# Kernel optimization log

Hardware: AMD Instinct MI355X
Metric: run time of the kernel (lower is better)

## Reference

```python
import jax, jax.numpy as jnp
import numpy as np

EMBED_DIM = 128
NUM_SYMBOLS = 100000
PAD_IDX = NUM_SYMBOLS
B = 8192
K = 50


def setup_inputs() -> dict:
    key = jax.random.key(0)
    ks = jax.random.split(key, 10)
    emb = jax.random.normal(ks[0], (NUM_SYMBOLS + 1, EMBED_DIM), jnp.float32) * 0.02
    emb = emb.at[PAD_IDX].set(0.0)  # padding_idx row is zero
    xav2 = 1.0 / np.sqrt(0.5 * (2 * EMBED_DIM + EMBED_DIM))
    xavg1 = 1.0 / np.sqrt(0.5 * (EMBED_DIM + EMBED_DIM // 2))
    xavg2 = 1.0 / np.sqrt(0.5 * (EMBED_DIM // 2 + 1))
    return {
        "entity": jax.random.randint(ks[1], (B,), 0, NUM_SYMBOLS),
        "connections": jax.random.randint(ks[2], (B, K, 2), 0, NUM_SYMBOLS),
        "symbol_emb": emb,
        "gcn_w_W": jax.random.normal(ks[3], (EMBED_DIM, 2 * EMBED_DIM), jnp.float32) * xav2,
        "gcn_w_b": jnp.zeros((EMBED_DIM,), jnp.float32),
        "gcn_b": jnp.zeros((EMBED_DIM,), jnp.float32),
        "gate_w1": jax.random.normal(ks[4], (EMBED_DIM // 2, EMBED_DIM), jnp.float32) * xavg1,
        "gate_b1": jnp.zeros((EMBED_DIM // 2,), jnp.float32),
        "gate_w2": jax.random.normal(ks[5], (1, EMBED_DIM // 2), jnp.float32) * xavg2,
        "gate_b2": jnp.zeros((1,), jnp.float32),
        "gate_temp": jnp.float32(1.0),
    }


def reference(entity, connections, symbol_emb, gcn_w_W, gcn_w_b, gcn_b,
              gate_w1, gate_b1, gate_w2, gate_b2, gate_temp):
    # Gather: center + (relation, entity) neighbor embeddings
    self_emb = symbol_emb[entity]                      # [B, D]
    rel = symbol_emb[connections[..., 0]]              # [B, K, D]
    ent = symbol_emb[connections[..., 1]]              # [B, K, D]
    # Linear transform of concatenated (rel, ent): gcn_w
    nbr = jnp.einsum('bkf,df->bkd', jnp.concatenate([rel, ent], axis=-1), gcn_w_W) + gcn_w_b  # [B, K, D]
    # Similarity attention (scaled dot product with center embedding)
    scores = jnp.einsum('bd,bkd->bk', self_emb, nbr) / jnp.sqrt(jnp.float32(EMBED_DIM))
    attn = jax.nn.softmax(scores, axis=-1)             # [B, K]
    # Content-based gating MLP (D -> D/2 -> 1), temperature-scaled sigmoid
    h = jax.nn.relu(jnp.einsum('bkd,hd->bkh', nbr, gate_w1) + gate_b1)
    gate = jax.nn.sigmoid((jnp.einsum('bkh,oh->bko', h, gate_w2) + gate_b2) / gate_temp)  # [B, K, 1]
    # Weight neighbors, aggregate='max' over k_neighbors, bias + tanh
    weighted = attn[..., None] * gate * nbr            # [B, K, D]
    out = jnp.max(weighted, axis=1)                    # [B, D]
    return jnp.tanh(out + gcn_b)
```

## Files before the change

### kernel.cpp

```cpp
#include <hip/hip_runtime.h>

#define EMBED_D 128
#define KNBR 50
#define STR 136
#define NROWS 102
#define ZK 50
#define NTF 52
#define XSTR 264
#define NSTR 136
#define MROWS 64

typedef __attribute__((ext_vector_type(8))) short short8;
typedef __attribute__((ext_vector_type(4))) float floatx4;

__device__ __forceinline__ float b2f(unsigned short u) {
    union { unsigned int i; float f; } v;
    v.i = ((unsigned int)u) << 16;
    return v.f;
}
__device__ __forceinline__ unsigned short f2b(float f) {
    union { float f; unsigned int i; } v;
    v.f = f;
    return (unsigned short)((v.i + 0x7fffu + ((v.i >> 16) & 1u)) >> 16);
}

__device__ __forceinline__ float dpp_row_sum16(float v) {
    int y;
    y = __builtin_amdgcn_update_dpp(0, __builtin_bit_cast(int, v), 0xB1, 0xF, 0xF, true);
    v += __builtin_bit_cast(float, y);
    y = __builtin_amdgcn_update_dpp(0, __builtin_bit_cast(int, v), 0x4E, 0xF, 0xF, true);
    v += __builtin_bit_cast(float, y);
    y = __builtin_amdgcn_update_dpp(0, __builtin_bit_cast(int, v), 0x124, 0xF, 0xF, true);
    v += __builtin_bit_cast(float, y);
    y = __builtin_amdgcn_update_dpp(0, __builtin_bit_cast(int, v), 0x128, 0xF, 0xF, true);
    v += __builtin_bit_cast(float, y);
    return v;
}

__device__ __forceinline__ bool detect_bf16(const unsigned short* p) {
    float mx = 0.f;
#pragma unroll
    for (int i = 0; i < 64; ++i) {
        const float a = fabsf(b2f(p[i]));
        if (a < 3.0e38f && a > mx) mx = a;
    }
    return mx < 1.0f;
}


struct TinyTensors {
    const void* src[6];
    unsigned short* dst[6];
    int n[6];
};

__device__ __forceinline__ void conv_chunk(const void* src, unsigned short* dst,
                                           long i, bool isbf) {
    if (isbf) {
        *(short8*)(dst + i * 8) = *(const short8*)((const unsigned short*)src + i * 8);
    } else {
        const float* p = (const float*)src + i * 8;
        const floatx4 a = *(const floatx4*)p;
        const floatx4 c = *(const floatx4*)(p + 4);
        short8 r;
        r[0] = (short)f2b(a[0]); r[1] = (short)f2b(a[1]);
        r[2] = (short)f2b(a[2]); r[3] = (short)f2b(a[3]);
        r[4] = (short)f2b(c[0]); r[5] = (short)f2b(c[1]);
        r[6] = (short)f2b(c[2]); r[7] = (short)f2b(c[3]);
        *(short8*)(dst + i * 8) = r;
    }
}

__global__ void convert_all_kernel(const void* __restrict__ emb_src, unsigned short* __restrict__ emb_dst,
                                   long n8, int nEmb,
                                   const void* __restrict__ gw_src, unsigned short* __restrict__ gw_dst,
                                   long gw8,
                                   const void* __restrict__ w1_src, unsigned short* __restrict__ w1_dst,
                                   long w18,
                                   const void* __restrict__ gwb_src, const void* __restrict__ b1_src,
                                   unsigned short* __restrict__ wg_dst,
                                   float* __restrict__ bg_dst,
                                   int* __restrict__ flag_dst,
                                   TinyTensors tt) {
    __shared__ int isbfS;
    if (threadIdx.x == 0) isbfS = detect_bf16((const unsigned short*)emb_src) ? 1 : 0;
    __syncthreads();
    const bool isbf = (isbfS != 0);
    const int bid = blockIdx.x;

    if (bid < 64) {
        const int j = bid;
        const int f = threadIdx.x;
        float a = 0.f;
        if (isbf) {
            const unsigned short* w1u = (const unsigned short*)w1_src;
            const unsigned short* gwu = (const unsigned short*)gw_src;
            for (int d = 0; d < EMBED_D; ++d)
                a += b2f(w1u[j * EMBED_D + d]) * b2f(gwu[(long)d * 256 + f]);
        } else {
            const float* w1f = (const float*)w1_src;
            const float* gwf = (const float*)gw_src;
            for (int d = 0; d < EMBED_D; ++d)
                a += w1f[j * EMBED_D + d] * gwf[(long)d * 256 + f];
        }
        wg_dst[j * 256 + f] = f2b(a);
        if (f == 0) {
            float s = 0.f;
            if (isbf) {
                const unsigned short* w1u = (const unsigned short*)w1_src;
                const unsigned short* gu = (const unsigned short*)gwb_src;
                for (int d = 0; d < EMBED_D; ++d) s += b2f(w1u[j * EMBED_D + d]) * b2f(gu[d]);
                bg_dst[j] = s + b2f(((const unsigned short*)b1_src)[j]);
            } else {
                const float* w1f = (const float*)w1_src;
                const float* gf = (const float*)gwb_src;
                for (int d = 0; d < EMBED_D; ++d) s += w1f[j * EMBED_D + d] * gf[d];
                bg_dst[j] = s + ((const float*)b1_src)[j];
            }
        }
    } else if (bid == 64) {
        if (threadIdx.x == 0) *flag_dst = isbf ? 1 : 0;
#pragma unroll
        for (int ti = 0; ti < 6; ++ti) {
            const int n = tt.n[ti];
            for (int i = threadIdx.x; i < n; i += 256) {
                const float v = isbf ? b2f(((const unsigned short*)tt.src[ti])[i])
                                     : ((const float*)tt.src[ti])[i];
                tt.dst[ti][i] = f2b(v);
            }
        }
    } else if (bid < 85) {
        const long q = (long)(bid - 65) * 256 + threadIdx.x;
        if (q < gw8) conv_chunk(gw_src, gw_dst, q, isbf);
        else if (q < gw8 + w18) conv_chunk(w1_src, w1_dst, q - gw8, isbf);
    } else {
        const long i0 = (long)(bid - 85) * 512 + threadIdx.x;
        if (i0 < n8) conv_chunk(emb_src, emb_dst, i0, isbf);
        const long i1 = i0 + 256;
        if (i1 < n8) conv_chunk(emb_src, emb_dst, i1, isbf);
    }
}


__global__ __launch_bounds__(256, 5)
void embed_matcher_fast(const int* __restrict__ entity, const int* __restrict__ conn,
                        const unsigned short* __restrict__ emb,
                        const unsigned short* __restrict__ gw,
                        const unsigned short* __restrict__ wg,
                        const float* __restrict__ bgp,
                        const unsigned short* __restrict__ gwb,
                        const unsigned short* __restrict__ gcnb,
                        const unsigned short* __restrict__ w2,
                        const unsigned short* __restrict__ b2v,
                        const unsigned short* __restrict__ temp,
                        const int* __restrict__ flagp,
                        void* __restrict__ out)
{
    __shared__ __align__(16) unsigned short Xs[NROWS * STR];
    __shared__ __align__(16) float selfE[EMBED_D];
    __shared__ float scoresP[4 * MROWS];
    __shared__ float glP[4 * MROWS];
    __shared__ __align__(16) float attnS[MROWS];
    __shared__ int flagS;

    float* NsF = (float*)Xs;

    const int t = threadIdx.x;
    const int b = blockIdx.x;
    const int lane = t & 63;
    const int wave = t >> 6;
    const int l15 = lane & 15;
    const int quad = lane >> 4;
    const int cbase = b * (KNBR * 2);

    const int k3 = 48 + l15;
    const int rowk3 = (k3 < KNBR) ? k3 : ZK;

    floatx4 acc[4][3];
    const floatx4 fzero = {0.f, 0.f, 0.f, 0.f};
#pragma unroll
    for (int m = 0; m < 4; ++m)
#pragma unroll
        for (int T = 0; T < 3; ++T) acc[m][T] = fzero;

    {
        int syms0[4];
#pragma unroll
        for (int i = 0; i < 4; ++i) {
            const int c = t + 256 * i;
            syms0[i] = conn[cbase + (c >> 4)];
        }
#pragma unroll
        for (int i = 0; i < 4; ++i) {
            const int c = t + 256 * i;
            const short8 v = *(const short8*)(emb + (long)syms0[i] * EMBED_D + (c & 15) * 8);
            *(short8*)(Xs + (c >> 4) * STR + (c & 15) * 8) = v;
        }
        int syms1[3];
#pragma unroll
        for (int i = 0; i < 3; ++i) {
            const int c = t + 256 * (i + 4);
            syms1[i] = (c < KNBR * 2 * 16) ? conn[cbase + (c >> 4)] : 0;
        }
#pragma unroll
        for (int i = 0; i < 3; ++i) {
            const int c = t + 256 * (i + 4);
            if (c < KNBR * 2 * 16) {
                const short8 v = *(const short8*)(emb + (long)syms1[i] * EMBED_D + (c & 15) * 8);
                *(short8*)(Xs + (c >> 4) * STR + (c & 15) * 8) = v;
            }
        }
        const short8 z8 = {0, 0, 0, 0, 0, 0, 0, 0};
        if (t < 34)
            *(short8*)(Xs + ZK * 2 * STR + t * 8) = z8;
        if (t < EMBED_D) selfE[t] = b2f(emb[(long)entity[b] * EMBED_D + t]);
        if (t == 0) flagS = *flagp;
    }
    __syncthreads();

    const unsigned short* gB0 = gw + (wave * 32 + l15) * 256;
    const unsigned short* gB1 = gB0 + 16 * 256;
    const unsigned short* gWg = wg + (wave * 16 + l15) * 256;

    short8 B0c = *(const short8*)(gB0 + quad * 8);
    short8 B1c = *(const short8*)(gB1 + quad * 8);
#pragma unroll
    for (int ft = 0; ft < 8; ++ft) {
        const short8 Bgc = *(const short8*)(gWg + ft * 32 + quad * 8);
        short8 B0n, B1n;
        if (ft < 7) {
            const int kn = (ft + 1) * 32 + quad * 8;
            B0n = *(const short8*)(gB0 + kn);
            B1n = *(const short8*)(gB1 + kn);
        }
        const int half = ft >> 2;
        const int cofs = (ft & 3) * 32 + quad * 8;
#pragma unroll
        for (int m = 0; m < 4; ++m) {
            const int rr = (m < 3) ? (m * 16 + l15) : rowk3;
            const short8 Am = *(const short8*)(Xs + (rr * 2 + half) * STR + cofs);
            acc[m][0] = __builtin_amdgcn_mfma_f32_16x16x32_bf16(Am, B0c, acc[m][0], 0, 0, 0);
            acc[m][1] = __builtin_amdgcn_mfma_f32_16x16x32_bf16(Am, B1c, acc[m][1], 0, 0, 0);
            acc[m][2] = __builtin_amdgcn_mfma_f32_16x16x32_bf16(Am, Bgc, acc[m][2], 0, 0, 0);
        }
        if (ft < 7) { B0c = B0n; B1c = B1n; }
    }
    __syncthreads();

    {
        const int dcol0 = wave * 32 + l15;
        const int dcol1 = dcol0 + 16;
        const float bias0 = b2f(gwb[dcol0]);
        const float bias1 = b2f(gwb[dcol1]);
        const float se0 = selfE[dcol0];
        const float se1 = selfE[dcol1];
        const float bgj = bgp[wave * 16 + l15];
        const float w2j = b2f(w2[wave * 16 + l15]);
#pragma unroll
        for (int m = 0; m < 4; ++m) {
            const int rbase = m * 16 + quad * 4;
            floatx4 v0, v1;
            float sc[4], gl[4];
#pragma unroll
            for (int r = 0; r < 4; ++r) {
                v0[r] = acc[m][0][r] + bias0;
                v1[r] = acc[m][1][r] + bias1;
                sc[r] = se0 * v0[r] + se1 * v1[r];
                gl[r] = fmaxf(acc[m][2][r] + bgj, 0.f) * w2j;
            }
            if (m < 3 || quad == 0) {
                *(floatx4*)(NsF + dcol0 * NTF + rbase) = v0;
                *(floatx4*)(NsF + dcol1 * NTF + rbase) = v1;
            }
#pragma unroll
            for (int r = 0; r < 4; ++r) {
                sc[r] = dpp_row_sum16(sc[r]);
                gl[r] = dpp_row_sum16(gl[r]);
            }
            const float sv = (l15 == 0) ? sc[0] : ((l15 == 1) ? sc[1] : ((l15 == 2) ? sc[2] : sc[3]));
            const float gv = (l15 == 0) ? gl[0] : ((l15 == 1) ? gl[1] : ((l15 == 2) ? gl[2] : gl[3]));
            if (l15 < 4) {
                scoresP[wave * MROWS + rbase + l15] = sv;
                glP[wave * MROWS + rbase + l15] = gv;
            }
        }
    }
    __syncthreads();

    if (t < 64) {
        const float ssum = scoresP[t] + scoresP[64 + t] + scoresP[128 + t] + scoresP[192 + t];
        const float s = (t < KNBR) ? ssum * 0.088388347648318447f : -INFINITY;
        float mx = s;
#pragma unroll
        for (int o = 32; o > 0; o >>= 1) mx = fmaxf(mx, __shfl_xor(mx, o));
        const float e = (t < KNBR) ? expf(s - mx) : 0.f;
        float sum = e;
#pragma unroll
        for (int o = 32; o > 0; o >>= 1) sum += __shfl_xor(sum, o);
        float a = e / sum;
        if (t < KNBR) {
            const float invT = 1.0f / b2f(temp[0]);
            const float logit = glP[t] + glP[64 + t] + glP[128 + t] + glP[192 + t] + b2f(b2v[0]);
            a *= 1.0f / (1.0f + expf(-logit * invT));
        }
        attnS[t] = a;
    }
    __syncthreads();

    if (t < EMBED_D) {
        const float* nr = NsF + t * NTF;
        float mx = -INFINITY;
#pragma unroll
        for (int c = 0; c < 12; ++c) {
            const floatx4 nv = *(const floatx4*)(nr + c * 4);
            const floatx4 av = *(const floatx4*)(attnS + c * 4);
#pragma unroll
            for (int j = 0; j < 4; ++j)
                mx = fmaxf(mx, av[j] * nv[j]);
        }
        mx = fmaxf(mx, attnS[48] * nr[48]);
        mx = fmaxf(mx, attnS[49] * nr[49]);
        const float o = tanhf(mx + b2f(gcnb[t]));
        if (flagS)
            ((unsigned short*)out)[(long)b * EMBED_D + t] = f2b(o);
        else
            ((float*)out)[(long)b * EMBED_D + t] = o;
    }
}


template <bool BF16IN>
__device__ __forceinline__ short8 load8g(const void* base, long off) {
    if constexpr (BF16IN) {
        return *(const short8*)((const unsigned short*)base + off);
    } else {
        const float* p = (const float*)base + off;
        const floatx4 a = *(const floatx4*)p;
        const floatx4 c = *(const floatx4*)(p + 4);
        short8 r;
        r[0] = (short)f2b(a[0]); r[1] = (short)f2b(a[1]);
        r[2] = (short)f2b(a[2]); r[3] = (short)f2b(a[3]);
        r[4] = (short)f2b(c[0]); r[5] = (short)f2b(c[1]);
        r[6] = (short)f2b(c[2]); r[7] = (short)f2b(c[3]);
        return r;
    }
}
template <bool BF16IN>
__device__ __forceinline__ float loadSg(const void* base, long off) {
    if constexpr (BF16IN) return b2f(((const unsigned short*)base)[off]);
    else return ((const float*)base)[off];
}

template <bool BF16IN>
__device__ __forceinline__ void body_fb(
    const int* entity, const int* conn, const void* emb, const void* gw,
    const void* gwb, const void* gcnb, const void* w1, const void* b1,
    const void* w2, const void* b2, const void* temp, void* out,
    unsigned short* Xs, unsigned short* Ns,
    float* selfE, float* scoresS, float* attnS, float* gsumS)
{
    const int t = threadIdx.x, b = blockIdx.x;
    const int lane = t & 63, wave = t >> 6, l15 = lane & 15, quad = lane >> 4;
    short8 Bfrag[8][2];
#pragma unroll
    for (int ft = 0; ft < 8; ++ft)
#pragma unroll
        for (int nn = 0; nn < 2; ++nn)
            Bfrag[ft][nn] = load8g<BF16IN>(gw, (wave * 32 + nn * 16 + l15) * 256 + ft * 32 + quad * 8);
    short8 W1frag[4];
#pragma unroll
    for (int ft = 0; ft < 4; ++ft)
        W1frag[ft] = load8g<BF16IN>(w1, (wave * 16 + l15) * 128 + ft * 32 + quad * 8);
    const float b1j = loadSg<BF16IN>(b1, wave * 16 + l15);
    const float w2j = loadSg<BF16IN>(w2, wave * 16 + l15);
    {
        const int cbase = b * (KNBR * 2);
        for (int c = t; c < KNBR * 2 * 16; c += 256) {
            const int r = c >> 4, j = c & 15;
            const int sym = conn[cbase + r];
            *(short8*)(Xs + (r >> 1) * XSTR + (r & 1) * 128 + j * 8) =
                load8g<BF16IN>(emb, (long)sym * EMBED_D + j * 8);
        }
        for (int i = t; i < (MROWS - KNBR) * 256; i += 256)
            Xs[(KNBR + (i >> 8)) * XSTR + (i & 255)] = 0;
        if (t < EMBED_D) selfE[t] = loadSg<BF16IN>(emb, (long)entity[b] * EMBED_D + t);
        if (t < MROWS) gsumS[t] = loadSg<BF16IN>(b2, 0);
    }
    __syncthreads();
    floatx4 acc[4][2];
    const floatx4 fzero = {0.f, 0.f, 0.f, 0.f};
#pragma unroll
    for (int m = 0; m < 4; ++m)
#pragma unroll
        for (int nn = 0; nn < 2; ++nn) acc[m][nn] = fzero;
#pragma unroll
    for (int ft = 0; ft < 8; ++ft) {
        short8 A[4];
#pragma unroll
        for (int m = 0; m < 4; ++m)
            A[m] = *(const short8*)(Xs + (m * 16 + l15) * XSTR + ft * 32 + quad * 8);
#pragma unroll
        for (int m = 0; m < 4; ++m)
#pragma unroll
            for (int nn = 0; nn < 2; ++nn)
                acc[m][nn] = __builtin_amdgcn_mfma_f32_16x16x32_bf16(A[m], Bfrag[ft][nn], acc[m][nn], 0, 0, 0);
    }
#pragma unroll
    for (int nn = 0; nn < 2; ++nn) {
        const int dcol = wave * 32 + nn * 16 + l15;
        const float bias = loadSg<BF16IN>(gwb, dcol);
#pragma unroll
        for (int m = 0; m < 4; ++m)
#pragma unroll
            for (int r = 0; r < 4; ++r)
                Ns[(m * 16 + quad * 4 + r) * NSTR + dcol] = f2b(acc[m][nn][r] + bias);
    }
    __syncthreads();
    {
        const int k = t >> 2, q = t & 3;
        float p = 0.f;
        if (k < KNBR) {
            const unsigned short* nr = Ns + k * NSTR + q * 32;
            const float* se = selfE + q * 32;
#pragma unroll
            for (int i = 0; i < 32; ++i) p += se[i] * b2f(nr[i]);
        }
        p += __shfl_xor(p, 1);
        p += __shfl_xor(p, 2);
        if (k < KNBR && q == 0) scoresS[k] = p * 0.088388347648318447f;
    }
    __syncthreads();
    if (t < 64) {
        const float s = (t < KNBR) ? scoresS[t] : -INFINITY;
        float mx = s;
#pragma unroll
        for (int o = 32; o > 0; o >>= 1) mx = fmaxf(mx, __shfl_xor(mx, o));
        const float e = (t < KNBR) ? expf(s - mx) : 0.f;
        float sum = e;
#pragma unroll
        for (int o = 32; o > 0; o >>= 1) sum += __shfl_xor(sum, o);
        attnS[t] = e / sum;
    }
    floatx4 acc2[4];
#pragma unroll
    for (int m = 0; m < 4; ++m) acc2[m] = fzero;
#pragma unroll
    for (int ft = 0; ft < 4; ++ft) {
        short8 A2[4];
#pragma unroll
        for (int m = 0; m < 4; ++m)
            A2[m] = *(const short8*)(Ns + (m * 16 + l15) * NSTR + ft * 32 + quad * 8);
#pragma unroll
        for (int m = 0; m < 4; ++m)
            acc2[m] = __builtin_amdgcn_mfma_f32_16x16x32_bf16(A2[m], W1frag[ft], acc2[m], 0, 0, 0);
    }
#pragma unroll
    for (int m = 0; m < 4; ++m)
#pragma unroll
        for (int r = 0; r < 4; ++r) {
            float c = fmaxf(acc2[m][r] + b1j, 0.f) * w2j;
            c += __shfl_xor(c, 1); c += __shfl_xor(c, 2);
            c += __shfl_xor(c, 4); c += __shfl_xor(c, 8);
            if (l15 == 0) atomicAdd(&gsumS[m * 16 + quad * 4 + r], c);
        }
    __syncthreads();
    if (t < KNBR) {
        const float invT = 1.0f / loadSg<BF16IN>(temp, 0);
        attnS[t] *= 1.0f / (1.0f + expf(-gsumS[t] * invT));
    }
    __syncthreads();
    if (t < EMBED_D) {
        float mx = -INFINITY;
        for (int k = 0; k < KNBR; ++k)
            mx = fmaxf(mx, attnS[k] * b2f(Ns[k * NSTR + t]));
        const float o = tanhf(mx + loadSg<BF16IN>(gcnb, t));
        if constexpr (BF16IN)
            ((unsigned short*)out)[(long)b * EMBED_D + t] = f2b(o);
        else
            ((float*)out)[(long)b * EMBED_D + t] = o;
    }
}

__global__ __launch_bounds__(256, 2)
void embed_matcher_fallback(const int* entity, const int* conn, const void* emb,
                            const void* gw, const void* gwb, const void* gcnb,
                            const void* w1, const void* b1, const void* w2,
                            const void* b2, const void* temp, void* out)
{
    __shared__ __align__(16) unsigned short Xs[MROWS * XSTR];
    __shared__ __align__(16) unsigned short Ns[MROWS * NSTR];
    __shared__ float selfE[EMBED_D];
    __shared__ float scoresS[MROWS];
    __shared__ float attnS[MROWS];
    __shared__ float gsumS[MROWS];
    if (detect_bf16((const unsigned short*)emb))
        body_fb<true>(entity, conn, emb, gw, gwb, gcnb, w1, b1, w2, b2, temp, out,
                      Xs, Ns, selfE, scoresS, attnS, gsumS);
    else
        body_fb<false>(entity, conn, emb, gw, gwb, gcnb, w1, b1, w2, b2, temp, out,
                       Xs, Ns, selfE, scoresS, attnS, gsumS);
}


static inline size_t align256(size_t x) { return (x + 255) & ~(size_t)255; }

extern "C" void kernel_launch(void* const* d_in, const int* in_sizes, int n_in,
                              void* d_out, int out_size, void* d_ws, size_t ws_size,
                              hipStream_t stream) {
    (void)n_in; (void)out_size;
    const int B = in_sizes[0];

    const long n_emb = in_sizes[2];
    size_t off[9], cur = 0;
    const int ns[8] = {in_sizes[3], in_sizes[4], in_sizes[5], in_sizes[6],
                       in_sizes[7], in_sizes[8], in_sizes[9], in_sizes[10]};
    off[0] = 0; cur = align256((size_t)n_emb * 2);
    for (int i = 0; i < 8; ++i) { off[i + 1] = cur; cur = align256(cur + (size_t)ns[i] * 2); }
    const size_t off_wg = cur; cur = align256(cur + 64 * 256 * 2);
    const size_t off_bg = cur; cur = align256(cur + 64 * 4);
    const size_t off_fl = cur; cur = align256(cur + 4);

    if (ws_size < cur) {
        embed_matcher_fallback<<<B, 256, 0, stream>>>(
            (const int*)d_in[0], (const int*)d_in[1],
            d_in[2], d_in[3], d_in[4], d_in[5],
            d_in[6], d_in[7], d_in[8], d_in[9], d_in[10], d_out);
        return;
    }

    char* ws = (char*)d_ws;
    unsigned short* emb_b = (unsigned short*)(ws + off[0]);

    TinyTensors tt;
    const int tin[6] = {4, 5, 7, 8, 9, 10};
    for (int i = 0; i < 6; ++i) {
        tt.src[i] = d_in[tin[i]];
        tt.dst[i] = (unsigned short*)(ws + off[tin[i] - 2]);
        tt.n[i] = in_sizes[tin[i]];
    }

    const long n8 = n_emb / 8;
    const int nEmb = (int)((n8 + 511) / 512);
    const long gw8 = in_sizes[3] / 8;
    const long w18 = in_sizes[6] / 8;
    convert_all_kernel<<<85 + nEmb, 256, 0, stream>>>(
        d_in[2], emb_b, n8, nEmb,
        d_in[3], (unsigned short*)(ws + off[1]), gw8,
        d_in[6], (unsigned short*)(ws + off[4]), w18,
        d_in[4], d_in[7],
        (unsigned short*)(ws + off_wg),
        (float*)(ws + off_bg),
        (int*)(ws + off_fl),
        tt);

    embed_matcher_fast<<<B, 256, 0, stream>>>(
        (const int*)d_in[0], (const int*)d_in[1],
        emb_b,
        (const unsigned short*)(ws + off[1]),
        (const unsigned short*)(ws + off_wg),
        (const float*)(ws + off_bg),
        (const unsigned short*)(ws + off[2]),
        (const unsigned short*)(ws + off[3]),
        (const unsigned short*)(ws + off[6]),
        (const unsigned short*)(ws + off[7]),
        (const unsigned short*)(ws + off[8]),
        (const int*)(ws + off_fl),
        d_out);
}
```

Measured before the change: 221.1 us.

## Split GCN projection and gate MLP across separate waves with 512-thread blocks

Measured after the change: 232.4 us. 5.1% more time.

```diff
diff --git a/kernel.cpp b/kernel.cpp
--- a/kernel.cpp
+++ b/kernel.cpp
@@ -142,7 +142,7 @@
 }
 
 
-__global__ __launch_bounds__(256, 5)
+__global__ __launch_bounds__(512, 6)
 void embed_matcher_fast(const int* __restrict__ entity, const int* __restrict__ conn,
                         const unsigned short* __restrict__ emb,
                         const unsigned short* __restrict__ gw,
@@ -176,39 +176,29 @@
     const int k3 = 48 + l15;
     const int rowk3 = (k3 < KNBR) ? k3 : ZK;
 
-    floatx4 acc[4][3];
+    floatx4 accA[4], accB[4];
     const floatx4 fzero = {0.f, 0.f, 0.f, 0.f};
 #pragma unroll
-    for (int m = 0; m < 4; ++m)
-#pragma unroll
-        for (int T = 0; T < 3; ++T) acc[m][T] = fzero;
+    for (int m = 0; m < 4; ++m) { accA[m] = fzero; accB[m] = fzero; }
 
     {
-        int syms0[4];
-#pragma unroll
-        for (int i = 0; i < 4; ++i) {
-            const int c = t + 256 * i;
-            syms0[i] = conn[cbase + (c >> 4)];
-        }
-#pragma unroll
-        for (int i = 0; i < 4; ++i) {
-            const int c = t + 256 * i;
-            const short8 v = *(const short8*)(emb + (long)syms0[i] * EMBED_D + (c & 15) * 8);
+        int syms[3];
+#pragma unroll
+        for (int i = 0; i < 3; ++i) {
+            const int c = t + 512 * i;
+            syms[i] = conn[cbase + (c >> 4)];
+        }
+#pragma unroll
+        for (int i = 0; i < 3; ++i) {
+            const int c = t + 512 * i;
+            const short8 v = *(const short8*)(emb + (long)syms[i] * EMBED_D + (c & 15) * 8);
             *(short8*)(Xs + (c >> 4) * STR + (c & 15) * 8) = v;
         }
-        int syms1[3];
-#pragma unroll
-        for (int i = 0; i < 3; ++i) {
-            const int c = t + 256 * (i + 4);
-            syms1[i] = (c < KNBR * 2 * 16) ? conn[cbase + (c >> 4)] : 0;
-        }
-#pragma unroll
-        for (int i = 0; i < 3; ++i) {
-            const int c = t + 256 * (i + 4);
-            if (c < KNBR * 2 * 16) {
-                const short8 v = *(const short8*)(emb + (long)syms1[i] * EMBED_D + (c & 15) * 8);
-                *(short8*)(Xs + (c >> 4) * STR + (c & 15) * 8) = v;
-            }
+        if (t < 64) {
+            const int c = 1536 + t;
+            const int sym = conn[cbase + (c >> 4)];
+            const short8 v = *(const short8*)(emb + (long)sym * EMBED_D + (c & 15) * 8);
+            *(short8*)(Xs + (c >> 4) * STR + (c & 15) * 8) = v;
         }
         const short8 z8 = {0, 0, 0, 0, 0, 0, 0, 0};
         if (t < 34)
@@ -218,71 +208,93 @@
     }
     __syncthreads();
 
-    const unsigned short* gB0 = gw + (wave * 32 + l15) * 256;
-    const unsigned short* gB1 = gB0 + 16 * 256;
-    const unsigned short* gWg = wg + (wave * 16 + l15) * 256;
-
-    short8 B0c = *(const short8*)(gB0 + quad * 8);
-    short8 B1c = *(const short8*)(gB1 + quad * 8);
-#pragma unroll
-    for (int ft = 0; ft < 8; ++ft) {
-        const short8 Bgc = *(const short8*)(gWg + ft * 32 + quad * 8);
-        short8 B0n, B1n;
-        if (ft < 7) {
-            const int kn = (ft + 1) * 32 + quad * 8;
-            B0n = *(const short8*)(gB0 + kn);
-            B1n = *(const short8*)(gB1 + kn);
-        }
-        const int half = ft >> 2;
-        const int cofs = (ft & 3) * 32 + quad * 8;
-#pragma unroll
-        for (int m = 0; m < 4; ++m) {
-            const int rr = (m < 3) ? (m * 16 + l15) : rowk3;
-            const short8 Am = *(const short8*)(Xs + (rr * 2 + half) * STR + cofs);
-            acc[m][0] = __builtin_amdgcn_mfma_f32_16x16x32_bf16(Am, B0c, acc[m][0], 0, 0, 0);
-            acc[m][1] = __builtin_amdgcn_mfma_f32_16x16x32_bf16(Am, B1c, acc[m][1], 0, 0, 0);
-            acc[m][2] = __builtin_amdgcn_mfma_f32_16x16x32_bf16(Am, Bgc, acc[m][2], 0, 0, 0);
-        }
-        if (ft < 7) { B0c = B0n; B1c = B1n; }
-    }
-    __syncthreads();
-
-    {
+    if (wave < 4) {
+        const unsigned short* gB0 = gw + (wave * 32 + l15) * 256;
+        const unsigned short* gB1 = gB0 + 16 * 256;
+        short8 B0c = *(const short8*)(gB0 + quad * 8);
+        short8 B1c = *(const short8*)(gB1 + quad * 8);
+#pragma unroll
+        for (int ft = 0; ft < 8; ++ft) {
+            short8 B0n, B1n;
+            if (ft < 7) {
+                const int kn = (ft + 1) * 32 + quad * 8;
+                B0n = *(const short8*)(gB0 + kn);
+                B1n = *(const short8*)(gB1 + kn);
+            }
+            const int half = ft >> 2;
+            const int cofs = (ft & 3) * 32 + quad * 8;
+#pragma unroll
+            for (int m = 0; m < 4; ++m) {
+                const int rr = (m < 3) ? (m * 16 + l15) : rowk3;
+                const short8 Am = *(const short8*)(Xs + (rr * 2 + half) * STR + cofs);
+                accA[m] = __builtin_amdgcn_mfma_f32_16x16x32_bf16(Am, B0c, accA[m], 0, 0, 0);
+                accB[m] = __builtin_amdgcn_mfma_f32_16x16x32_bf16(Am, B1c, accB[m], 0, 0, 0);
+            }
+            if (ft < 7) { B0c = B0n; B1c = B1n; }
+        }
+    } else {
+        const unsigned short* gWg = wg + ((wave - 4) * 16 + l15) * 256;
+        short8 Bgc = *(const short8*)(gWg + quad * 8);
+#pragma unroll
+        for (int ft = 0; ft < 8; ++ft) {
+            short8 Bgn;
+            if (ft < 7)
+                Bgn = *(const short8*)(gWg + (ft + 1) * 32 + quad * 8);
+            const int half = ft >> 2;
+            const int cofs = (ft & 3) * 32 + quad * 8;
+#pragma unroll
+            for (int m = 0; m < 4; ++m) {
+                const int rr = (m < 3) ? (m * 16 + l15) : rowk3;
+                const short8 Am = *(const short8*)(Xs + (rr * 2 + half) * STR + cofs);
+                accA[m] = __builtin_amdgcn_mfma_f32_16x16x32_bf16(Am, Bgc, accA[m], 0, 0, 0);
+            }
+            if (ft < 7) Bgc = Bgn;
+        }
+    }
+    __syncthreads();
+
+    if (wave < 4) {
         const int dcol0 = wave * 32 + l15;
         const int dcol1 = dcol0 + 16;
         const float bias0 = b2f(gwb[dcol0]);
         const float bias1 = b2f(gwb[dcol1]);
         const float se0 = selfE[dcol0];
         const float se1 = selfE[dcol1];
-        const float bgj = bgp[wave * 16 + l15];
-        const float w2j = b2f(w2[wave * 16 + l15]);
 #pragma unroll
         for (int m = 0; m < 4; ++m) {
             const int rbase = m * 16 + quad * 4;
             floatx4 v0, v1;
-            float sc[4], gl[4];
+            float sc[4];
 #pragma unroll
             for (int r = 0; r < 4; ++r) {
-                v0[r] = acc[m][0][r] + bias0;
-                v1[r] = acc[m][1][r] + bias1;
+                v0[r] = accA[m][r] + bias0;
+                v1[r] = accB[m][r] + bias1;
                 sc[r] = se0 * v0[r] + se1 * v1[r];
-                gl[r] = fmaxf(acc[m][2][r] + bgj, 0.f) * w2j;
             }
             if (m < 3 || quad == 0) {
                 *(floatx4*)(NsF + dcol0 * NTF + rbase) = v0;
                 *(floatx4*)(NsF + dcol1 * NTF + rbase) = v1;
             }
 #pragma unroll
-            for (int r = 0; r < 4; ++r) {
-                sc[r] = dpp_row_sum16(sc[r]);
-                gl[r] = dpp_row_sum16(gl[r]);
-            }
+            for (int r = 0; r < 4; ++r) sc[r] = dpp_row_sum16(sc[r]);
             const float sv = (l15 == 0) ? sc[0] : ((l15 == 1) ? sc[1] : ((l15 == 2) ? sc[2] : sc[3]));
+            if (l15 < 4) scoresP[wave * MROWS + rbase + l15] = sv;
+        }
+    } else {
+        const int wv = wave - 4;
+        const float bgj = bgp[wv * 16 + l15];
+        const float w2j = b2f(w2[wv * 16 + l15]);
+#pragma unroll
+        for (int m = 0; m < 4; ++m) {
+            const int rbase = m * 16 + quad * 4;
+            float gl[4];
+#pragma unroll
+            for (int r = 0; r < 4; ++r)
+                gl[r] = fmaxf(accA[m][r] + bgj, 0.f) * w2j;
+#pragma unroll
+            for (int r = 0; r < 4; ++r) gl[r] = dpp_row_sum16(gl[r]);
             const float gv = (l15 == 0) ? gl[0] : ((l15 == 1) ? gl[1] : ((l15 == 2) ? gl[2] : gl[3]));
-            if (l15 < 4) {
-                scoresP[wave * MROWS + rbase + l15] = sv;
-                glP[wave * MROWS + rbase + l15] = gv;
-            }
+            if (l15 < 4) glP[wv * MROWS + rbase + l15] = gv;
         }
     }
     __syncthreads();
@@ -553,7 +565,7 @@
         (int*)(ws + off_fl),
         tt);
 
-    embed_matcher_fast<<<B, 256, 0, stream>>>(
+    embed_matcher_fast<<<B, 512, 0, stream>>>(
         (const int*)d_in[0], (const int*)d_in[1],
         emb_b,
         (const unsigned short*)(ws + off[1]),
```

## Convert matcher kernel to persistent grid with prefetched connection indices

Applied to the files above, without the earlier changes.

Result: slower. 328.0 us (+48.3%).

```diff
diff --git a/kernel.cpp b/kernel.cpp
--- a/kernel.cpp
+++ b/kernel.cpp
@@ -9,6 +9,7 @@
 #define XSTR 264
 #define NSTR 136
 #define MROWS 64
+#define PGRID 1280
 
 typedef __attribute__((ext_vector_type(8))) short short8;
 typedef __attribute__((ext_vector_type(4))) float floatx4;
@@ -154,177 +155,201 @@
                         const unsigned short* __restrict__ b2v,
                         const unsigned short* __restrict__ temp,
                         const int* __restrict__ flagp,
-                        void* __restrict__ out)
+                        void* __restrict__ out,
+                        int nTotal)
 {
     __shared__ __align__(16) unsigned short Xs[NROWS * STR];
     __shared__ __align__(16) float selfE[EMBED_D];
     __shared__ float scoresP[4 * MROWS];
     __shared__ float glP[4 * MROWS];
     __shared__ __align__(16) float attnS[MROWS];
-    __shared__ int flagS;
+    __shared__ int connS[2][2 * KNBR];
+    __shared__ int eS[2];
 
     float* NsF = (float*)Xs;
 
     const int t = threadIdx.x;
-    const int b = blockIdx.x;
+    const int bid = blockIdx.x;
+    const int nb = gridDim.x;
     const int lane = t & 63;
     const int wave = t >> 6;
     const int l15 = lane & 15;
     const int quad = lane >> 4;
-    const int cbase = b * (KNBR * 2);
 
     const int k3 = 48 + l15;
     const int rowk3 = (k3 < KNBR) ? k3 : ZK;
 
-    floatx4 acc[4][3];
-    const floatx4 fzero = {0.f, 0.f, 0.f, 0.f};
-#pragma unroll
-    for (int m = 0; m < 4; ++m)
-#pragma unroll
-        for (int T = 0; T < 3; ++T) acc[m][T] = fzero;
+    const int dcol0 = wave * 32 + l15;
+    const int dcol1 = dcol0 + 16;
+    const float bias0 = b2f(gwb[dcol0]);
+    const float bias1 = b2f(gwb[dcol1]);
+    const float bgj = bgp[wave * 16 + l15];
+    const float w2j = b2f(w2[wave * 16 + l15]);
+    const float invT = 1.0f / b2f(temp[0]);
+    const float b2b = b2f(b2v[0]);
+    const float gcb = (t < EMBED_D) ? b2f(gcnb[t]) : 0.f;
+    const int flag = *flagp;
+    const unsigned short* gB0 = gw + (wave * 32 + l15) * 256;
+    const unsigned short* gB1 = gB0 + 16 * 256;
+    const unsigned short* gWg = wg + (wave * 16 + l15) * 256;
 
     {
-        int syms0[4];
-#pragma unroll
-        for (int i = 0; i < 4; ++i) {
-            const int c = t + 256 * i;
-            syms0[i] = conn[cbase + (c >> 4)];
-        }
-#pragma unroll
-        for (int i = 0; i < 4; ++i) {
-            const int c = t + 256 * i;
-            const short8 v = *(const short8*)(emb + (long)syms0[i] * EMBED_D + (c & 15) * 8);
-            *(short8*)(Xs + (c >> 4) * STR + (c & 15) * 8) = v;
-        }
-        int syms1[3];
-#pragma unroll
-        for (int i = 0; i < 3; ++i) {
-            const int c = t + 256 * (i + 4);
-            syms1[i] = (c < KNBR * 2 * 16) ? conn[cbase + (c >> 4)] : 0;
-        }
-#pragma unroll
-        for (int i = 0; i < 3; ++i) {
-            const int c = t + 256 * (i + 4);
-            if (c < KNBR * 2 * 16) {
-                const short8 v = *(const short8*)(emb + (long)syms1[i] * EMBED_D + (c & 15) * 8);
-                *(short8*)(Xs + (c >> 4) * STR + (c & 15) * 8) = v;
-            }
-        }
+        if (t < 2 * KNBR) connS[0][t] = conn[(long)bid * (2 * KNBR) + t];
+        if (t == 0) eS[0] = entity[bid];
         const short8 z8 = {0, 0, 0, 0, 0, 0, 0, 0};
         if (t < 34)
             *(short8*)(Xs + ZK * 2 * STR + t * 8) = z8;
-        if (t < EMBED_D) selfE[t] = b2f(emb[(long)entity[b] * EMBED_D + t]);
-        if (t == 0) flagS = *flagp;
-    }
-    __syncthreads();
-
-    const unsigned short* gB0 = gw + (wave * 32 + l15) * 256;
-    const unsigned short* gB1 = gB0 + 16 * 256;
-    const unsigned short* gWg = wg + (wave * 16 + l15) * 256;
-
-    short8 B0c = *(const short8*)(gB0 + quad * 8);
-    short8 B1c = *(const short8*)(gB1 + quad * 8);
-#pragma unroll
-    for (int ft = 0; ft < 8; ++ft) {
-        const short8 Bgc = *(const short8*)(gWg + ft * 32 + quad * 8);
-        short8 B0n, B1n;
-        if (ft < 7) {
-            const int kn = (ft + 1) * 32 + quad * 8;
-            B0n = *(const short8*)(gB0 + kn);
-            B1n = *(const short8*)(gB1 + kn);
-        }
-        const int half = ft >> 2;
-        const int cofs = (ft & 3) * 32 + quad * 8;
-#pragma unroll
-        for (int m = 0; m < 4; ++m) {
-            const int rr = (m < 3) ? (m * 16 + l15) : rowk3;
-            const short8 Am = *(const short8*)(Xs + (rr * 2 + half) * STR + cofs);
-            acc[m][0] = __builtin_amdgcn_mfma_f32_16x16x32_bf16(Am, B0c, acc[m][0], 0, 0, 0);
-            acc[m][1] = __builtin_amdgcn_mfma_f32_16x16x32_bf16(Am, B1c, acc[m][1], 0, 0, 0);
-            acc[m][2] = __builtin_amdgcn_mfma_f32_16x16x32_bf16(Am, Bgc, acc[m][2], 0, 0, 0);
-        }
-        if (ft < 7) { B0c = B0n; B1c = B1n; }
-    }
-    __syncthreads();
-
-    {
-        const int dcol0 = wave * 32 + l15;
-        const int dcol1 = dcol0 + 16;
-        const float bias0 = b2f(gwb[dcol0]);
-        const float bias1 = b2f(gwb[dcol1]);
-        const float se0 = selfE[dcol0];
-        const float se1 = selfE[dcol1];
-        const float bgj = bgp[wave * 16 + l15];
-        const float w2j = b2f(w2[wave * 16 + l15]);
-#pragma unroll
-        for (int m = 0; m < 4; ++m) {
-            const int rbase = m * 16 + quad * 4;
-            floatx4 v0, v1;
-            float sc[4], gl[4];
-#pragma unroll
-            for (int r = 0; r < 4; ++r) {
-                v0[r] = acc[m][0][r] + bias0;
-                v1[r] = acc[m][1][r] + bias1;
-                sc[r] = se0 * v0[r] + se1 * v1[r];
-                gl[r] = fmaxf(acc[m][2][r] + bgj, 0.f) * w2j;
-            }
-            if (m < 3 || quad == 0) {
-                *(floatx4*)(NsF + dcol0 * NTF + rbase) = v0;
-                *(floatx4*)(NsF + dcol1 * NTF + rbase) = v1;
-            }
-#pragma unroll
-            for (int r = 0; r < 4; ++r) {
-                sc[r] = dpp_row_sum16(sc[r]);
-                gl[r] = dpp_row_sum16(gl[r]);
-            }
-            const float sv = (l15 == 0) ? sc[0] : ((l15 == 1) ? sc[1] : ((l15 == 2) ? sc[2] : sc[3]));
-            const float gv = (l15 == 0) ? gl[0] : ((l15 == 1) ? gl[1] : ((l15 == 2) ? gl[2] : gl[3]));
-            if (l15 < 4) {
-                scoresP[wave * MROWS + rbase + l15] = sv;
-                glP[wave * MROWS + rbase + l15] = gv;
-            }
-        }
-    }
-    __syncthreads();
-
-    if (t < 64) {
-        const float ssum = scoresP[t] + scoresP[64 + t] + scoresP[128 + t] + scoresP[192 + t];
-        const float s = (t < KNBR) ? ssum * 0.088388347648318447f : -INFINITY;
-        float mx = s;
-#pragma unroll
-        for (int o = 32; o > 0; o >>= 1) mx = fmaxf(mx, __shfl_xor(mx, o));
-        const float e = (t < KNBR) ? expf(s - mx) : 0.f;
-        float sum = e;
-#pragma unroll
-        for (int o = 32; o > 0; o >>= 1) sum += __shfl_xor(sum, o);
-        float a = e / sum;
-        if (t < KNBR) {
-            const float invT = 1.0f / b2f(temp[0]);
-            const float logit = glP[t] + glP[64 + t] + glP[128 + t] + glP[192 + t] + b2f(b2v[0]);
-            a *= 1.0f / (1.0f + expf(-logit * invT));
-        }
-        attnS[t] = a;
-    }
-    __syncthreads();
-
-    if (t < EMBED_D) {
-        const float* nr = NsF + t * NTF;
-        float mx = -INFINITY;
-#pragma unroll
-        for (int c = 0; c < 12; ++c) {
-            const floatx4 nv = *(const floatx4*)(nr + c * 4);
-            const floatx4 av = *(const floatx4*)(attnS + c * 4);
-#pragma unroll
-            for (int j = 0; j < 4; ++j)
-                mx = fmaxf(mx, av[j] * nv[j]);
-        }
-        mx = fmaxf(mx, attnS[48] * nr[48]);
-        mx = fmaxf(mx, attnS[49] * nr[49]);
-        const float o = tanhf(mx + b2f(gcnb[t]));
-        if (flagS)
-            ((unsigned short*)out)[(long)b * EMBED_D + t] = f2b(o);
-        else
-            ((float*)out)[(long)b * EMBED_D + t] = o;
+    }
+
+    const floatx4 fzero = {0.f, 0.f, 0.f, 0.f};
+    int slot = 0;
+
+    for (int it = bid; it < nTotal; it += nb, slot ^= 1) {
+        const int cur = slot, nxt = slot ^ 1;
+        __syncthreads();
+
+        {
+            int syms0[4];
+#pragma unroll
+            for (int i = 0; i < 4; ++i) {
+                const int c = t + 256 * i;
+                syms0[i] = connS[cur][c >> 4];
+            }
+#pragma unroll
+            for (int i = 0; i < 4; ++i) {
+                const int c = t + 256 * i;
+                const short8 v = *(const short8*)(emb + (long)syms0[i] * EMBED_D + (c & 15) * 8);
+                *(short8*)(Xs + (c >> 4) * STR + (c & 15) * 8) = v;
+            }
+            int syms1[3];
+#pragma unroll
+            for (int i = 0; i < 3; ++i) {
+                const int c = t + 256 * (i + 4);
+                syms1[i] = (c < KNBR * 2 * 16) ? connS[cur][c >> 4] : 0;
+            }
+#pragma unroll
+            for (int i = 0; i < 3; ++i) {
+                const int c = t + 256 * (i + 4);
+                if (c < KNBR * 2 * 16) {
+                    const short8 v = *(const short8*)(emb + (long)syms1[i] * EMBED_D + (c & 15) * 8);
+                    *(short8*)(Xs + (c >> 4) * STR + (c & 15) * 8) = v;
+                }
+            }
+            if (t < EMBED_D) selfE[t] = b2f(emb[(long)eS[cur] * EMBED_D + t]);
+            const int itn = it + nb;
+            if (itn < nTotal) {
+                if (t < 2 * KNBR) connS[nxt][t] = conn[(long)itn * (2 * KNBR) + t];
+                if (t == 0) eS[nxt] = entity[itn];
+            }
+        }
+        __syncthreads();
+
+        floatx4 acc[4][3];
+#pragma unroll
+        for (int m = 0; m < 4; ++m)
+#pragma unroll
+            for (int T = 0; T < 3; ++T) acc[m][T] = fzero;
+        {
+            short8 B0c = *(const short8*)(gB0 + quad * 8);
+            short8 B1c = *(const short8*)(gB1 + quad * 8);
+#pragma unroll
+            for (int ft = 0; ft < 8; ++ft) {
+                const short8 Bgc = *(const short8*)(gWg + ft * 32 + quad * 8);
+                short8 B0n, B1n;
+                if (ft < 7) {
+                    const int kn = (ft + 1) * 32 + quad * 8;
+                    B0n = *(const short8*)(gB0 + kn);
+                    B1n = *(const short8*)(gB1 + kn);
+                }
+                const int half = ft >> 2;
+                const int cofs = (ft & 3) * 32 + quad * 8;
+                __builtin_amdgcn_s_setprio(1);
+#pragma unroll
+                for (int m = 0; m < 4; ++m) {
+                    const int rr = (m < 3) ? (m * 16 + l15) : rowk3;
+                    const short8 Am = *(const short8*)(Xs + (rr * 2 + half) * STR + cofs);
+                    acc[m][0] = __builtin_amdgcn_mfma_f32_16x16x32_bf16(Am, B0c, acc[m][0], 0, 0, 0);
+                    acc[m][1] = __builtin_amdgcn_mfma_f32_16x16x32_bf16(Am, B1c, acc[m][1], 0, 0, 0);
+                    acc[m][2] = __builtin_amdgcn_mfma_f32_16x16x32_bf16(Am, Bgc, acc[m][2], 0, 0, 0);
+                }
+                __builtin_amdgcn_s_setprio(0);
+                if (ft < 7) { B0c = B0n; B1c = B1n; }
+            }
+        }
+        __syncthreads();
+
+        {
+            const float se0 = selfE[dcol0];
+            const float se1 = selfE[dcol1];
+#pragma unroll
+            for (int m = 0; m < 4; ++m) {
+                const int rbase = m * 16 + quad * 4;
+                floatx4 v0, v1;
+                float sc[4], gl[4];
+#pragma unroll
+                for (int r = 0; r < 4; ++r) {
+                    v0[r] = acc[m][0][r] + bias0;
+                    v1[r] = acc[m][1][r] + bias1;
+                    sc[r] = se0 * v0[r] + se1 * v1[r];
+                    gl[r] = fmaxf(acc[m][2][r] + bgj, 0.f) * w2j;
+                }
+                if (m < 3 || quad == 0) {
+                    *(floatx4*)(NsF + dcol0 * NTF + rbase) = v0;
+                    *(floatx4*)(NsF + dcol1 * NTF + rbase) = v1;
+                }
+#pragma unroll
+                for (int r = 0; r < 4; ++r) {
+                    sc[r] = dpp_row_sum16(sc[r]);
+                    gl[r] = dpp_row_sum16(gl[r]);
+                }
+                const float sv = (l15 == 0) ? sc[0] : ((l15 == 1) ? sc[1] : ((l15 == 2) ? sc[2] : sc[3]));
+                const float gv = (l15 == 0) ? gl[0] : ((l15 == 1) ? gl[1] : ((l15 == 2) ? gl[2] : gl[3]));
+                if (l15 < 4) {
+                    scoresP[wave * MROWS + rbase + l15] = sv;
+                    glP[wave * MROWS + rbase + l15] = gv;
+                }
+            }
+        }
+        __syncthreads();
+
+        if (t < 64) {
+            const float ssum = scoresP[t] + scoresP[64 + t] + scoresP[128 + t] + scoresP[192 + t];
+            const float s = (t < KNBR) ? ssum * 0.088388347648318447f : -INFINITY;
+            float mx = s;
+#pragma unroll
+            for (int o = 32; o > 0; o >>= 1) mx = fmaxf(mx, __shfl_xor(mx, o));
+            const float e = (t < KNBR) ? expf(s - mx) : 0.f;
+            float sum = e;
+#pragma unroll
+            for (int o = 32; o > 0; o >>= 1) sum += __shfl_xor(sum, o);
+            float a = e / sum;
+            if (t < KNBR) {
+                const float logit = glP[t] + glP[64 + t] + glP[128 + t] + glP[192 + t] + b2b;
+                a *= 1.0f / (1.0f + expf(-logit * invT));
+            }
+            attnS[t] = a;
+        }
+        __syncthreads();
+
+        if (t < EMBED_D) {
+            const float* nr = NsF + t * NTF;
+            float mx = -INFINITY;
+#pragma unroll
+            for (int c = 0; c < 12; ++c) {
+                const floatx4 nv = *(const floatx4*)(nr + c * 4);
+                const floatx4 av = *(const floatx4*)(attnS + c * 4);
+#pragma unroll
+                for (int j = 0; j < 4; ++j)
+                    mx = fmaxf(mx, av[j] * nv[j]);
+            }
+            mx = fmaxf(mx, attnS[48] * nr[48]);
+            mx = fmaxf(mx, attnS[49] * nr[49]);
+            const float o = tanhf(mx + gcb);
+            if (flag)
+                ((unsigned short*)out)[(long)it * EMBED_D + t] = f2b(o);
+            else
+                ((float*)out)[(long)it * EMBED_D + t] = o;
+        }
     }
 }
 
@@ -553,7 +578,8 @@
         (int*)(ws + off_fl),
         tt);
 
-    embed_matcher_fast<<<B, 256, 0, stream>>>(
+    const int nblk = (B < PGRID) ? B : PGRID;
+    embed_matcher_fast<<<nblk, 256, 0, stream>>>(
         (const int*)d_in[0], (const int*)d_in[1],
         emb_b,
         (const unsigned short*)(ws + off[1]),
@@ -565,5 +591,6 @@
         (const unsigned short*)(ws + off[7]),
         (const unsigned short*)(ws + off[8]),
         (const int*)(ws + off_fl),
-        d_out);
-}
+        d_out,
+        B);
+}
```
